# Optimization experiments

Hardware: AMD Instinct MI355X
Metric: run time of the kernel (lower is better)

The kernel has to match this reference:

```python
import jax, jax.numpy as jnp
import numpy as np

NUM_HEADS = 16
HEAD_SIZE = 64
LN_EPS = 1e-5


def setup_inputs() -> dict:
    key = jax.random.key(0)
    k1, k2, k3 = jax.random.split(key, 3)
    b, l, hidden = 2, 2048, 1024
    qkv_out = HEAD_SIZE * NUM_HEADS + 2 * HEAD_SIZE  # 1152
    x = jax.random.normal(k1, (b, l, hidden), dtype=jnp.float32)
    Wqkv = jax.random.normal(k2, (qkv_out, hidden), dtype=jnp.float32) * 0.02
    gamma = jnp.ones((qkv_out,), dtype=jnp.float32)
    beta = jnp.zeros((qkv_out,), dtype=jnp.float32)
    Wfc = jax.random.normal(k3, (hidden, HEAD_SIZE * NUM_HEADS), dtype=jnp.float32) * 0.02
    return {"x": x, "Wqkv": Wqkv, "gamma": gamma, "beta": beta, "Wfc": Wfc}


def reference(x, Wqkv, gamma, beta, Wfc):
    h, d = NUM_HEADS, HEAD_SIZE
    b, l, _ = x.shape
    # fused QKV projection (no bias), then LayerNorm over the FULL qkv dim
    qkv = jnp.einsum('blc,oc->blo', x, Wqkv)  # (b, l, (h+2)*d)
    mu = jnp.mean(qkv, axis=-1, keepdims=True)
    var = jnp.var(qkv, axis=-1, keepdims=True)
    qkv = (qkv - mu) * jax.lax.rsqrt(var + LN_EPS) * gamma + beta
    qkv = qkv.reshape(b, l, h + 2, d)
    k = qkv[:, :, 0, :]       # (b, l, d) shared K head
    v = qkv[:, :, 1, :]       # (b, l, d) shared V head
    q = qkv[:, :, 2:, :]      # (b, l, h, d) query heads
    scale = 1.0 / np.sqrt(d).astype(np.float32)
    scores = jnp.einsum('bqhd,bkd->bhqk', q, k) * scale  # (b, h, l, l)
    causal = jnp.tril(jnp.ones((l, l), dtype=bool))
    scores = jnp.where(causal, scores, jnp.finfo(scores.dtype).min)
    attn = jax.nn.softmax(scores, axis=-1)
    out = jnp.einsum('bhqk,bkd->bqhd', attn, v).reshape(b, l, h * d)
    return jnp.einsum('blo,ho->blh', out, Wfc)
```

## Files before the change

### kernel.cpp

```cpp
#include <hip/hip_runtime.h>
#include <stdint.h>

typedef __attribute__((ext_vector_type(8))) short s16x8;
typedef __attribute__((ext_vector_type(4))) float f32x4;

#define MFMA16(a, b, c) __builtin_amdgcn_mfma_f32_16x16x32_bf16((a), (b), (c), 0, 0, 0)

__device__ __forceinline__ unsigned short f2bf(float f) {
    unsigned int u = __float_as_uint(f);
    return (unsigned short)((u + 0x7FFFu + ((u >> 16) & 1u)) >> 16);
}
__device__ __forceinline__ float bf2f(unsigned short h) {
    return __uint_as_float(((unsigned int)h) << 16);
}
__device__ __forceinline__ void cvt8(unsigned short* dst, const float* src) {
    const float4 f0 = *(const float4*)(src);
    const float4 f1 = *(const float4*)(src + 4);
    s16x8 v;
    v[0] = (short)f2bf(f0.x); v[1] = (short)f2bf(f0.y);
    v[2] = (short)f2bf(f0.z); v[3] = (short)f2bf(f0.w);
    v[4] = (short)f2bf(f1.x); v[5] = (short)f2bf(f1.y);
    v[6] = (short)f2bf(f1.z); v[7] = (short)f2bf(f1.w);
    *(s16x8*)dst = v;
}
__device__ __forceinline__ void gl_lds16(const unsigned short* g, unsigned short* l) {
    __builtin_amdgcn_global_load_lds(
        (const __attribute__((address_space(1))) unsigned int*)g,
        (__attribute__((address_space(3))) unsigned int*)l,
        16, 0, 0);
}

__global__ __launch_bounds__(256) void cvt_all(const float* __restrict__ x,
                                               const float* __restrict__ wq,
                                               const float* __restrict__ wf,
                                               unsigned short* __restrict__ xb,
                                               unsigned short* __restrict__ wqb,
                                               unsigned short* __restrict__ wfb) {
    const int blk = blockIdx.x;
    const float* src;
    unsigned short* dst;
    int base;
    if (blk < 2048)      { src = x;  dst = xb;  base = blk; }
    else if (blk < 2624) { src = wq; dst = wqb; base = blk - 2048; }
    else                 { src = wf; dst = wfb; base = blk - 2624; }
    const int i = (base * 256 + threadIdx.x) * 8;
    cvt8(&dst[i], &src[i]);
}

template <bool OUT_F32>
__global__ __launch_bounds__(512) void gemm_mn(const unsigned short* __restrict__ A,
                                               const unsigned short* __restrict__ Bw,
                                               void* __restrict__ Cout, int K, int N) {
    const int bm = blockIdx.x, bn = blockIdx.y;
    const int t = threadIdx.x;
    const int lane = t & 63, w = t >> 6;
    const int quad = lane >> 4, col = lane & 15;
    const int wm = (w >> 1) * 32, wn = (w & 1) * 32;

    __shared__ alignas(16) unsigned short As[2][128 * 64];
    __shared__ alignas(16) unsigned short Bs[2][64 * 64];

    f32x4 acc[2][2];
#pragma unroll
    for (int i = 0; i < 2; ++i)
#pragma unroll
        for (int j = 0; j < 2; ++j) acc[i][j] = (f32x4){0.f, 0.f, 0.f, 0.f};

    const int lrow = lane >> 3;
    const int lcol = ((lane & 7) ^ lrow) * 8;
    const unsigned short* Ap = A + (size_t)(bm * 128 + w * 16 + lrow) * K + lcol;
    const unsigned short* Bp = Bw + (size_t)(bn * 64 + w * 8 + lrow) * K + lcol;

#pragma unroll
    for (int j = 0; j < 2; ++j)
        gl_lds16(Ap + (size_t)(j * 8) * K, &As[0][(w * 16 + j * 8) * 64]);
    gl_lds16(Bp, &Bs[0][(w * 8) * 64]);
    __syncthreads();

    const int c7 = col & 7;
    const int fs0 = ((0 * 4 + quad) ^ c7) * 8;
    const int fs1 = ((1 * 4 + quad) ^ c7) * 8;

    for (int k0 = 0; k0 < K; k0 += 64) {
        const int p = (k0 >> 6) & 1;
        if (k0 + 64 < K) {
#pragma unroll
            for (int j = 0; j < 2; ++j)
                gl_lds16(Ap + (size_t)(j * 8) * K + k0 + 64, &As[p ^ 1][(w * 16 + j * 8) * 64]);
            gl_lds16(Bp + k0 + 64, &Bs[p ^ 1][(w * 8) * 64]);
        }
        s16x8 af[2][2], bfr[2][2];
#pragma unroll
        for (int s = 0; s < 2; ++s) {
            const int fs = s ? fs1 : fs0;
#pragma unroll
            for (int i = 0; i < 2; ++i)
                af[s][i] = *(const s16x8*)&As[p][(wm + i * 16 + col) * 64 + fs];
#pragma unroll
            for (int j = 0; j < 2; ++j)
                bfr[s][j] = *(const s16x8*)&Bs[p][(wn + j * 16 + col) * 64 + fs];
        }
#pragma unroll
        for (int s = 0; s < 2; ++s)
#pragma unroll
            for (int i = 0; i < 2; ++i)
#pragma unroll
                for (int j = 0; j < 2; ++j)
                    acc[i][j] = MFMA16(af[s][i], bfr[s][j], acc[i][j]);
        __syncthreads();
    }
    const int rowb = bm * 128 + wm + quad * 4;
    const int colb = bn * 64 + wn + col;
#pragma unroll
    for (int i = 0; i < 2; ++i)
#pragma unroll
        for (int j = 0; j < 2; ++j)
#pragma unroll
            for (int r = 0; r < 4; ++r) {
                size_t off = (size_t)(rowb + i * 16 + r) * N + colb + j * 16;
                if (OUT_F32) ((float*)Cout)[off] = acc[i][j][r];
                else ((unsigned short*)Cout)[off] = f2bf(acc[i][j][r]);
            }
}

__global__ __launch_bounds__(64) void ln_row(unsigned short* __restrict__ qkvn,
                                             const float* __restrict__ gamma,
                                             const float* __restrict__ beta,
                                             unsigned short* __restrict__ vT) {
    const int row = blockIdx.x;
    const int b = row >> 11, l = row & 2047;
    unsigned short* rp = qkvn + (size_t)row * 1152;
    const int lane = threadIdx.x;

    s16x8 v0 = *(const s16x8*)&rp[lane * 8];
    s16x8 v1 = *(const s16x8*)&rp[512 + lane * 8];
    unsigned int v2u = *(const unsigned int*)&rp[1024 + lane * 2];

    float f0[8], f1[8], f2[2];
    float s = 0.f, s2 = 0.f;
#pragma unroll
    for (int e = 0; e < 8; ++e) {
        f0[e] = bf2f((unsigned short)v0[e]);
        f1[e] = bf2f((unsigned short)v1[e]);
        s += f0[e] + f1[e];
        s2 += f0[e] * f0[e] + f1[e] * f1[e];
    }
    f2[0] = bf2f((unsigned short)(v2u & 0xFFFF));
    f2[1] = bf2f((unsigned short)(v2u >> 16));
    s += f2[0] + f2[1];
    s2 += f2[0] * f2[0] + f2[1] * f2[1];

#pragma unroll
    for (int off = 1; off < 64; off <<= 1) {
        s += __shfl_xor(s, off);
        s2 += __shfl_xor(s2, off);
    }
    const float mu = s * (1.0f / 1152.0f);
    float var = s2 * (1.0f / 1152.0f) - mu * mu;
    var = fmaxf(var, 0.0f);
    const float rstd = rsqrtf(var + 1e-5f);

    {
        s16x8 o;
#pragma unroll
        for (int e = 0; e < 8; ++e)
            o[e] = (short)f2bf((f0[e] - mu) * rstd * gamma[lane * 8 + e] + beta[lane * 8 + e]);
        *(s16x8*)&rp[lane * 8] = o;
        if (lane >= 8 && lane < 16) {
            const int d0 = lane * 8 - 64;
#pragma unroll
            for (int e = 0; e < 8; ++e)
                vT[((size_t)(b * 64 + d0 + e)) * 2048 + l] = (unsigned short)o[e];
        }
    }
    {
        s16x8 o;
#pragma unroll
        for (int e = 0; e < 8; ++e)
            o[e] = (short)f2bf((f1[e] - mu) * rstd * gamma[512 + lane * 8 + e] + beta[512 + lane * 8 + e]);
        *(s16x8*)&rp[512 + lane * 8] = o;
    }
    {
        unsigned short o0 = f2bf((f2[0] - mu) * rstd * gamma[1024 + lane * 2] + beta[1024 + lane * 2]);
        unsigned short o1 = f2bf((f2[1] - mu) * rstd * gamma[1025 + lane * 2] + beta[1025 + lane * 2]);
        *(unsigned int*)&rp[1024 + lane * 2] = ((unsigned int)o1 << 16) | o0;
    }
}

__global__ __launch_bounds__(512, 4) void attn_kernel(const unsigned short* __restrict__ qkvn,
                                                      const unsigned short* __restrict__ vT,
                                                      unsigned short* __restrict__ obuf) {
    const int b = blockIdx.x >> 3, hp = blockIdx.x & 7;
    const int yy = blockIdx.y;
    const int qb = (yy < 16) ? (31 - yy) : (yy - 16);
    const int t = threadIdx.x;
    const int lane = t & 63, w = t >> 6;
    const int quad = lane >> 4, col = lane & 15;
    const int hl = w >> 2;
    const int qhalf = (w >> 1) & 1;
    const int kpar = w & 1;

    __shared__ alignas(16) unsigned char SM[53248];
    unsigned short* Ks0 = (unsigned short*)SM;
    unsigned short* Vt0 = (unsigned short*)(SM + 16384);
    unsigned short* Qs  = (unsigned short*)(SM + 32768);
    unsigned short* Ps  = (unsigned short*)(SM + 32768) + w * 1280;

    const int srow = t >> 3;
    const int schunk = t & 7;
    const int ldsoff = srow * 64 + (schunk ^ (srow & 7)) * 8;

#pragma unroll
    for (int hh = 0; hh < 2; ++hh) {
        const unsigned short* qsrc =
            qkvn + (size_t)(b * 2048 + qb * 64 + srow) * 1152 + 128 + (hp * 2 + hh) * 64 + schunk * 8;
        s16x8 v = *(const s16x8*)qsrc;
#pragma unroll
        for (int e = 0; e < 8; ++e)
            v[e] = (short)f2bf(bf2f((unsigned short)v[e]) * 0.125f);
        *(s16x8*)&Qs[(hh * 64 + srow) * 80 + schunk * 8] = v;
    }
    __syncthreads();
    s16x8 qfr[2][2];
#pragma unroll
    for (int qf = 0; qf < 2; ++qf)
#pragma unroll
        for (int dh = 0; dh < 2; ++dh)
            qfr[qf][dh] = *(const s16x8*)&Qs[(hl * 64 + qhalf * 32 + qf * 16 + col) * 80 + dh * 32 + quad * 8];

    const unsigned short* kbase = qkvn + (size_t)(b * 2048 + srow) * 1152 + schunk * 8;
    const unsigned short* vbase = vT + (size_t)(b * 64 + srow) * 2048 + schunk * 8;
    *(uint4*)&Ks0[ldsoff] = *(const uint4*)(kbase);
    *(uint4*)&Vt0[ldsoff] = *(const uint4*)(vbase);
    __syncthreads();

    const int c7 = col & 7;
    const int koff0 = (kpar * 32 + col) * 128 + ((quad ^ c7) * 16);
    const int koff1 = (kpar * 32 + col) * 128 + (((4 + quad) ^ c7) * 16);
    const int voff = col * 128 + (((kpar * 4 + quad) ^ c7) * 16);

    s16x8 ones;
#pragma unroll
    for (int e = 0; e < 8; ++e) ones[e] = (short)0x3F80;

    f32x4 Oacc[4][2];
    f32x4 lacc[2];
#pragma unroll
    for (int ds = 0; ds < 4; ++ds)
#pragma unroll
        for (int qf = 0; qf < 2; ++qf) Oacc[ds][qf] = (f32x4){0.f, 0.f, 0.f, 0.f};
    lacc[0] = (f32x4){0.f, 0.f, 0.f, 0.f};
    lacc[1] = (f32x4){0.f, 0.f, 0.f, 0.f};

    const int qbase = qb * 64 + qhalf * 32;

    for (int kb = 0; kb <= qb; ++kb) {
        const int p = kb & 1;
        uint4 kreg, vreg;
        if (kb < qb) {
            kreg = *(const uint4*)(kbase + (size_t)(kb + 1) * 64 * 1152);
            vreg = *(const uint4*)(vbase + (kb + 1) * 64);
        }
        const bool diag = (kb == qb);
        if (!(diag && kpar == 1 && qhalf == 0)) {
            const bool needmask = diag && (kpar == qhalf);
            const char* kb8 = (const char*)(Ks0 + p * 4096);
            const char* vb8 = (const char*)(Vt0 + p * 4096);

#pragma unroll
            for (int nt = 0; nt < 2; ++nt) {
                const s16x8 kf0 = *(const s16x8*)(kb8 + nt * 2048 + koff0);
                const s16x8 kf1 = *(const s16x8*)(kb8 + nt * 2048 + koff1);
#pragma unroll
                for (int qf = 0; qf < 2; ++qf) {
                    f32x4 z = (f32x4){-12.f, -12.f, -12.f, -12.f};
                    z = MFMA16(kf0, qfr[qf][0], z);
                    z = MFMA16(kf1, qfr[qf][1], z);
                    const int qg = qbase + qf * 16 + col;
                    const int kl = kb * 64 + kpar * 32 + nt * 16 + quad * 4;
                    float ev[4];
#pragma unroll
                    for (int r = 0; r < 4; ++r) {
                        float sv = z[r];
                        if (needmask && (kl + r > qg)) sv = -1e30f;
                        ev[r] = __expf(sv);
                    }
                    unsigned int plo, phi;
                    asm("v_cvt_pk_bf16_f32 %0, %1, %2" : "=v"(plo) : "v"(ev[0]), "v"(ev[1]));
                    asm("v_cvt_pk_bf16_f32 %0, %1, %2" : "=v"(phi) : "v"(ev[2]), "v"(ev[3]));
                    uint2 pk2;
                    pk2.x = plo; pk2.y = phi;
                    *(uint2*)&Ps[(qf * 16 + col) * 40 + nt * 16 + quad * 4] = pk2;
                }
            }

            const s16x8 pf0 = *(const s16x8*)&Ps[col * 40 + quad * 8];
            const s16x8 pf1 = *(const s16x8*)&Ps[(16 + col) * 40 + quad * 8];
            __builtin_amdgcn_s_setprio(1);
            lacc[0] = MFMA16(ones, pf0, lacc[0]);
            lacc[1] = MFMA16(ones, pf1, lacc[1]);
#pragma unroll
            for (int ds = 0; ds < 4; ++ds) {
                const s16x8 vf = *(const s16x8*)(vb8 + ds * 2048 + voff);
                Oacc[ds][0] = MFMA16(vf, pf0, Oacc[ds][0]);
                Oacc[ds][1] = MFMA16(vf, pf1, Oacc[ds][1]);
            }
            __builtin_amdgcn_s_setprio(0);
        }

        if (kb < qb) {
            *(uint4*)&Ks0[(p ^ 1) * 4096 + ldsoff] = kreg;
            *(uint4*)&Vt0[(p ^ 1) * 4096 + ldsoff] = vreg;
        }
        __syncthreads();
    }

    float* mg = (float*)SM + (hl * 2 + qhalf) * 2112;
    float* lm = (float*)(SM + 33792) + (hl * 2 + qhalf) * 32;
    if (kpar) {
#pragma unroll
        for (int ds = 0; ds < 4; ++ds)
#pragma unroll
            for (int qf = 0; qf < 2; ++qf)
#pragma unroll
                for (int r = 0; r < 4; ++r)
                    mg[(ds * 16 + quad * 4 + r) * 33 + qf * 16 + col] = Oacc[ds][qf][r];
        if (quad == 0) { lm[col] = lacc[0][0]; lm[16 + col] = lacc[1][0]; }
    }
    __syncthreads();
    if (!kpar) {
        const int h = hp * 2 + hl;
#pragma unroll
        for (int qf = 0; qf < 2; ++qf) {
            const int qglob = qbase + qf * 16 + col;
            const float inv = 1.0f / (lacc[qf][0] + lm[qf * 16 + col]);
            const size_t base = (((size_t)b * 2048 + qglob) * 16 + h) * 64 + quad * 4;
#pragma unroll
            for (int ds = 0; ds < 4; ++ds) {
                ushort4 ov;
                unsigned short* op = (unsigned short*)&ov;
#pragma unroll
                for (int r = 0; r < 4; ++r)
                    op[r] = f2bf((Oacc[ds][qf][r] + mg[(ds * 16 + quad * 4 + r) * 33 + qf * 16 + col]) * inv);
                *(ushort4*)&obuf[base + ds * 16] = ov;
            }
        }
    }
}

extern "C" void kernel_launch(void* const* d_in, const int* in_sizes, int n_in,
                              void* d_out, int out_size, void* d_ws, size_t ws_size,
                              hipStream_t stream) {
    (void)in_sizes; (void)n_in; (void)out_size; (void)ws_size;
    const float* x     = (const float*)d_in[0];
    const float* Wqkv  = (const float*)d_in[1];
    const float* gamma = (const float*)d_in[2];
    const float* beta  = (const float*)d_in[3];
    const float* Wfc   = (const float*)d_in[4];
    float* out = (float*)d_out;

    char* ws = (char*)d_ws;
    unsigned short* xb   = (unsigned short*)ws;
    unsigned short* Wqb  = (unsigned short*)(ws + 8388608);
    unsigned short* Wfb  = (unsigned short*)(ws + 10747904);
    unsigned short* qkvn = (unsigned short*)(ws + 12845056);
    unsigned short* vT   = (unsigned short*)(ws + 22282240);
    unsigned short* abuf = (unsigned short*)ws;

    cvt_all<<<dim3(3136), 256, 0, stream>>>(x, Wqkv, Wfc, xb, Wqb, Wfb);
    gemm_mn<false><<<dim3(32, 18), 512, 0, stream>>>(xb, Wqb, qkvn, 1024, 1152);
    ln_row<<<dim3(4096), 64, 0, stream>>>(qkvn, gamma, beta, vT);
    attn_kernel<<<dim3(16, 32), 512, 0, stream>>>(qkvn, vT, abuf);
    gemm_mn<true><<<dim3(32, 16), 512, 0, stream>>>(abuf, Wfb, out, 1024, 1024);
}
```

Measured before the change: 145.0 us.

## Load K/V MFMA fragments directly from global memory, drop LDS staging and barriers

Stops staging K and V tiles through double-buffered LDS with a block barrier every key block. Each wave now reads its K and V fragments straight from global memory (expected to hit L2) into registers. Q fragments are also loaded and scaled directly, with no LDS round trip. The per-iteration __syncthreads goes away and LDS use drops, which may allow more resident blocks. In exchange every wave issues redundant uncoalesced global loads with no prefetch, so latency is exposed inside the loop.

```diff
diff --git a/kernel.cpp b/kernel.cpp
--- a/kernel.cpp
+++ b/kernel.cpp
@@ -200,44 +200,30 @@
     const int qhalf = (w >> 1) & 1;
     const int kpar = w & 1;
 
-    __shared__ alignas(16) unsigned char SM[53248];
-    unsigned short* Ks0 = (unsigned short*)SM;
-    unsigned short* Vt0 = (unsigned short*)(SM + 16384);
-    unsigned short* Qs  = (unsigned short*)(SM + 32768);
-    unsigned short* Ps  = (unsigned short*)(SM + 32768) + w * 1280;
-
-    const int srow = t >> 3;
-    const int schunk = t & 7;
-    const int ldsoff = srow * 64 + (schunk ^ (srow & 7)) * 8;
-
-#pragma unroll
-    for (int hh = 0; hh < 2; ++hh) {
-        const unsigned short* qsrc =
-            qkvn + (size_t)(b * 2048 + qb * 64 + srow) * 1152 + 128 + (hp * 2 + hh) * 64 + schunk * 8;
-        s16x8 v = *(const s16x8*)qsrc;
-#pragma unroll
-        for (int e = 0; e < 8; ++e)
-            v[e] = (short)f2bf(bf2f((unsigned short)v[e]) * 0.125f);
-        *(s16x8*)&Qs[(hh * 64 + srow) * 80 + schunk * 8] = v;
-    }
-    __syncthreads();
+    __shared__ alignas(16) unsigned char SM[34304];
+    unsigned short* Ps = (unsigned short*)SM + w * 1280;
+
+    const int h = hp * 2 + hl;
+
     s16x8 qfr[2][2];
 #pragma unroll
     for (int qf = 0; qf < 2; ++qf)
 #pragma unroll
-        for (int dh = 0; dh < 2; ++dh)
-            qfr[qf][dh] = *(const s16x8*)&Qs[(hl * 64 + qhalf * 32 + qf * 16 + col) * 80 + dh * 32 + quad * 8];
-
-    const unsigned short* kbase = qkvn + (size_t)(b * 2048 + srow) * 1152 + schunk * 8;
-    const unsigned short* vbase = vT + (size_t)(b * 64 + srow) * 2048 + schunk * 8;
-    *(uint4*)&Ks0[ldsoff] = *(const uint4*)(kbase);
-    *(uint4*)&Vt0[ldsoff] = *(const uint4*)(vbase);
-    __syncthreads();
-
-    const int c7 = col & 7;
-    const int koff0 = (kpar * 32 + col) * 128 + ((quad ^ c7) * 16);
-    const int koff1 = (kpar * 32 + col) * 128 + (((4 + quad) ^ c7) * 16);
-    const int voff = col * 128 + (((kpar * 4 + quad) ^ c7) * 16);
+        for (int dh = 0; dh < 2; ++dh) {
+            const unsigned short* qsrc =
+                qkvn + (size_t)(b * 2048 + qb * 64 + qhalf * 32 + qf * 16 + col) * 1152 +
+                128 + h * 64 + dh * 32 + quad * 8;
+            s16x8 v = *(const s16x8*)qsrc;
+#pragma unroll
+            for (int e = 0; e < 8; ++e)
+                v[e] = (short)f2bf(bf2f((unsigned short)v[e]) * 0.125f);
+            qfr[qf][dh] = v;
+        }
+
+    const unsigned short* kbase0 =
+        qkvn + (size_t)(b * 2048 + kpar * 32 + col) * 1152 + quad * 8;
+    const unsigned short* vbase0 =
+        vT + (size_t)(b * 64 + col) * 2048 + kpar * 32 + quad * 8;
 
     s16x8 ones;
 #pragma unroll
@@ -255,66 +241,57 @@
     const int qbase = qb * 64 + qhalf * 32;
 
     for (int kb = 0; kb <= qb; ++kb) {
-        const int p = kb & 1;
-        uint4 kreg, vreg;
-        if (kb < qb) {
-            kreg = *(const uint4*)(kbase + (size_t)(kb + 1) * 64 * 1152);
-            vreg = *(const uint4*)(vbase + (kb + 1) * 64);
-        }
         const bool diag = (kb == qb);
-        if (!(diag && kpar == 1 && qhalf == 0)) {
-            const bool needmask = diag && (kpar == qhalf);
-            const char* kb8 = (const char*)(Ks0 + p * 4096);
-            const char* vb8 = (const char*)(Vt0 + p * 4096);
-
-#pragma unroll
-            for (int nt = 0; nt < 2; ++nt) {
-                const s16x8 kf0 = *(const s16x8*)(kb8 + nt * 2048 + koff0);
-                const s16x8 kf1 = *(const s16x8*)(kb8 + nt * 2048 + koff1);
-#pragma unroll
-                for (int qf = 0; qf < 2; ++qf) {
-                    f32x4 z = (f32x4){-12.f, -12.f, -12.f, -12.f};
-                    z = MFMA16(kf0, qfr[qf][0], z);
-                    z = MFMA16(kf1, qfr[qf][1], z);
-                    const int qg = qbase + qf * 16 + col;
-                    const int kl = kb * 64 + kpar * 32 + nt * 16 + quad * 4;
-                    float ev[4];
-#pragma unroll
-                    for (int r = 0; r < 4; ++r) {
-                        float sv = z[r];
-                        if (needmask && (kl + r > qg)) sv = -1e30f;
-                        ev[r] = __expf(sv);
-                    }
-                    unsigned int plo, phi;
-                    asm("v_cvt_pk_bf16_f32 %0, %1, %2" : "=v"(plo) : "v"(ev[0]), "v"(ev[1]));
-                    asm("v_cvt_pk_bf16_f32 %0, %1, %2" : "=v"(phi) : "v"(ev[2]), "v"(ev[3]));
-                    uint2 pk2;
-                    pk2.x = plo; pk2.y = phi;
-                    *(uint2*)&Ps[(qf * 16 + col) * 40 + nt * 16 + quad * 4] = pk2;
+        if (diag && kpar == 1 && qhalf == 0) break;
+        const bool needmask = diag && (kpar == qhalf);
+
+        s16x8 vfr[4];
+#pragma unroll
+        for (int ds = 0; ds < 4; ++ds)
+            vfr[ds] = *(const s16x8*)(vbase0 + (size_t)(ds * 16) * 2048 + kb * 64);
+
+#pragma unroll
+        for (int nt = 0; nt < 2; ++nt) {
+            const unsigned short* krow = kbase0 + (size_t)(kb * 64 + nt * 16) * 1152;
+            const s16x8 kf0 = *(const s16x8*)(krow);
+            const s16x8 kf1 = *(const s16x8*)(krow + 32);
+#pragma unroll
+            for (int qf = 0; qf < 2; ++qf) {
+                f32x4 z = (f32x4){-12.f, -12.f, -12.f, -12.f};
+                z = MFMA16(kf0, qfr[qf][0], z);
+                z = MFMA16(kf1, qfr[qf][1], z);
+                const int qg = qbase + qf * 16 + col;
+                const int kl = kb * 64 + kpar * 32 + nt * 16 + quad * 4;
+                float ev[4];
+#pragma unroll
+                for (int r = 0; r < 4; ++r) {
+                    float sv = z[r];
+                    if (needmask && (kl + r > qg)) sv = -1e30f;
+                    ev[r] = __expf(sv);
                 }
+                unsigned int plo, phi;
+                asm("v_cvt_pk_bf16_f32 %0, %1, %2" : "=v"(plo) : "v"(ev[0]), "v"(ev[1]));
+                asm("v_cvt_pk_bf16_f32 %0, %1, %2" : "=v"(phi) : "v"(ev[2]), "v"(ev[3]));
+                uint2 pk2;
+                pk2.x = plo; pk2.y = phi;
+                *(uint2*)&Ps[(qf * 16 + col) * 40 + nt * 16 + quad * 4] = pk2;
             }
-
-            const s16x8 pf0 = *(const s16x8*)&Ps[col * 40 + quad * 8];
-            const s16x8 pf1 = *(const s16x8*)&Ps[(16 + col) * 40 + quad * 8];
-            __builtin_amdgcn_s_setprio(1);
-            lacc[0] = MFMA16(ones, pf0, lacc[0]);
-            lacc[1] = MFMA16(ones, pf1, lacc[1]);
-#pragma unroll
-            for (int ds = 0; ds < 4; ++ds) {
-                const s16x8 vf = *(const s16x8*)(vb8 + ds * 2048 + voff);
-                Oacc[ds][0] = MFMA16(vf, pf0, Oacc[ds][0]);
-                Oacc[ds][1] = MFMA16(vf, pf1, Oacc[ds][1]);
-            }
-            __builtin_amdgcn_s_setprio(0);
-        }
-
-        if (kb < qb) {
-            *(uint4*)&Ks0[(p ^ 1) * 4096 + ldsoff] = kreg;
-            *(uint4*)&Vt0[(p ^ 1) * 4096 + ldsoff] = vreg;
-        }
-        __syncthreads();
-    }
-
+        }
+
+        const s16x8 pf0 = *(const s16x8*)&Ps[col * 40 + quad * 8];
+        const s16x8 pf1 = *(const s16x8*)&Ps[(16 + col) * 40 + quad * 8];
+        __builtin_amdgcn_s_setprio(1);
+        lacc[0] = MFMA16(ones, pf0, lacc[0]);
+        lacc[1] = MFMA16(ones, pf1, lacc[1]);
+#pragma unroll
+        for (int ds = 0; ds < 4; ++ds) {
+            Oacc[ds][0] = MFMA16(vfr[ds], pf0, Oacc[ds][0]);
+            Oacc[ds][1] = MFMA16(vfr[ds], pf1, Oacc[ds][1]);
+        }
+        __builtin_amdgcn_s_setprio(0);
+    }
+
+    __syncthreads();
     float* mg = (float*)SM + (hl * 2 + qhalf) * 2112;
     float* lm = (float*)(SM + 33792) + (hl * 2 + qhalf) * 32;
     if (kpar) {
@@ -329,7 +306,6 @@
     }
     __syncthreads();
     if (!kpar) {
-        const int h = hp * 2 + hl;
 #pragma unroll
         for (int qf = 0; qf < 2; ++qf) {
             const int qglob = qbase + qf * 16 + col;
```

After: 181.6 us. +25.2%, slower.
